# Optimization experiments

Measured on AMD Instinct MI355X. Metric: run time of the kernel, lower is better.

## Reference

```python
import jax, jax.numpy as jnp
import numpy as np

B, S, DIN, DH, NB = 4, 2048, 256, 128, 50
LN_EPS = 1e-5
THRESHOLDS = (0.5, 1.0, 2.0, 4.0)


def _layernorm(x, g, b):
    m = jnp.mean(x, axis=-1, keepdims=True)
    v = jnp.mean((x - m) ** 2, axis=-1, keepdims=True)
    return (x - m) * jax.lax.rsqrt(v + LN_EPS) * g + b


def setup_inputs() -> dict:
    key = jax.random.key(0)
    ks = jax.random.split(key, 12)
    single_repr = jax.random.normal(ks[0], (B, S, DIN), jnp.float32)
    # coordinates spread out so the <=15A local neighborhood is nontrivial
    coordinates = jax.random.normal(ks[1], (B, S, 3), jnp.float32) * 12.0
    mask = jnp.ones((B, S), jnp.float32)
    sc = 0.05
    return {
        'single_repr': single_repr,
        'coordinates': coordinates,
        'mask': mask,
        'W1': jax.random.normal(ks[2], (DIN, DH), jnp.float32) * sc,
        'b1': jnp.zeros((DH,), jnp.float32),
        'g1': jnp.ones((DH,), jnp.float32),
        'be1': jnp.zeros((DH,), jnp.float32),
        'W2': jax.random.normal(ks[3], (DH, DH), jnp.float32) * sc,
        'b2': jnp.zeros((DH,), jnp.float32),
        'g2': jnp.ones((DH,), jnp.float32),
        'be2': jnp.zeros((DH,), jnp.float32),
        'W3': jax.random.normal(ks[4], (DH, NB), jnp.float32) * sc,
        'b3': jnp.zeros((NB,), jnp.float32),
        'temperature': jnp.ones((1,), jnp.float32),
    }


def reference(single_repr, coordinates, mask, W1, b1, g1, be1, W2, b2, g2, be2, W3, b3, temperature):
    # ---- confidence MLP (dropout in eval mode = identity) ----
    h = jax.nn.relu(_layernorm(single_repr @ W1 + b1, g1, be1))
    h = jax.nn.relu(_layernorm(h @ W2 + b2, g2, be2))
    logits = (h @ W3 + b3) / temperature          # [B, S, NB]
    probs = jax.nn.softmax(logits, axis=-1)

    # ---- vectorized pLDDT (replaces the per-residue Python loop) ----
    diff = coordinates[:, :, None, :] - coordinates[:, None, :, :]   # [B,S,S,3]
    D = jnp.sqrt(jnp.sum(diff * diff, axis=-1))                      # [B,S,S]
    maskb = mask > 0.0
    local = (D <= 15.0) & maskb[:, :, None] & maskb[:, None, :]      # [B,S,S]
    counts = jnp.sum(local, axis=-1).astype(jnp.float32)             # [B,S]
    frac_sum = jnp.zeros((B, S), jnp.float32)
    for t in THRESHOLDS:  # fixed small loop over 4 thresholds
        within = jnp.sum((D <= t) & local, axis=-1).astype(jnp.float32)
        frac_sum = frac_sum + within / jnp.maximum(counts, 1.0)
    plddt = jnp.where(counts > 0, frac_sum / len(THRESHOLDS) * 100.0, 0.0)

    # ---- final masking, as in torch forward ----
    plddt = plddt * mask
    logits_m = logits * mask[:, :, None]
    probs_m = probs * mask[:, :, None]
    return plddt, logits_m, probs_m
```

## Files before the change

kernel.cpp:

```cpp
#include <hip/hip_runtime.h>
#include <float.h>
#include <math.h>

#define B_   4
#define S_   2048
#define DIN_ 256
#define DH_  128
#define NB_  50
#define NBP_ 64
#define ROWS (B_ * S_)
#define MB   16

#define MLP_BLOCKS   (ROWS / MB)
#define PLDDT_ROWSPB 32
#define PLDDT_BLOCKS (ROWS / PLDDT_ROWSPB)

typedef __attribute__((ext_vector_type(8))) short  short8;
typedef __attribute__((ext_vector_type(4))) float  f32x4;

__device__ __forceinline__ unsigned short bf16_rne(float f) {
    unsigned u = __builtin_bit_cast(unsigned, f);
    u = u + 0x7fffu + ((u >> 16) & 1u);
    return (unsigned short)(u >> 16);
}

__global__ __launch_bounds__(256) void setup_w(
    const float* __restrict__ W1, const float* __restrict__ W2,
    const float* __restrict__ W3, unsigned short* __restrict__ wt)
{
    const int t = blockIdx.x * 256 + threadIdx.x;
    const int l = t & 63, m = l & 15, kg = l >> 4;
    float src[8];
    int dst;
    if (t < 4096) {
        const int c = t >> 6, nt = c >> 3, ks = c & 7;
        const int n = nt * 16 + m, k = ks * 32 + kg * 8;
#pragma unroll
        for (int i = 0; i < 8; ++i) src[i] = W1[(k + i) * DH_ + n];
        dst = t * 8;
    } else if (t < 6144) {
        const int s = t - 4096, c = s >> 6, nt = c >> 2, ks = c & 3;
        const int n = nt * 16 + m, k = ks * 32 + kg * 8;
#pragma unroll
        for (int i = 0; i < 8; ++i) src[i] = W2[(k + i) * DH_ + n];
        dst = 32768 + s * 8;
    } else {
        const int s = t - 6144, c = s >> 6, nt = c >> 2, ks = c & 3;
        const int n = nt * 16 + m, k = ks * 32 + kg * 8;
#pragma unroll
        for (int i = 0; i < 8; ++i) src[i] = (n < NB_) ? W3[(k + i) * NB_ + n] : 0.f;
        dst = 49152 + s * 8;
    }
    union { short8 v; unsigned short u[8]; } H;
#pragma unroll
    for (int i = 0; i < 8; ++i) H.u[i] = bf16_rne(src[i]);
    *(short8*)&wt[dst] = H.v;
}

union SharedU {
    struct {
        unsigned short sA[MB * DIN_];
        float sStats[MB][20];
        float sL[MB * NBP_];
    } mlp;
    f32x4 sP[S_];
};

__global__ __launch_bounds__(512) void fused_kernel(
    const float* __restrict__ x, const float* __restrict__ coords,
    const float* __restrict__ mask,
    const float* __restrict__ b1, const float* __restrict__ g1, const float* __restrict__ be1,
    const float* __restrict__ b2, const float* __restrict__ g2, const float* __restrict__ be2,
    const float* __restrict__ b3, const float* __restrict__ temp,
    const unsigned short* __restrict__ wt,
    float* __restrict__ out_plddt,
    float* __restrict__ out_logits, float* __restrict__ out_probs)
{
    __shared__ SharedU sh;
    const int tid  = threadIdx.x;
    const int lane = tid & 63;
    const int w    = tid >> 6;

    if (blockIdx.x < MLP_BLOCKS) {
        unsigned short* sA = sh.mlp.sA;
        const int m    = lane & 15;
        const int kg   = lane >> 4;
        const int row0 = blockIdx.x * MB;

        {
            const int r  = tid >> 5;
            const int kc = (tid & 31) << 3;
            const float* xp = x + (size_t)(row0 + r) * DIN_ + kc;
            f32x4 a = *(const f32x4*)xp;
            f32x4 b = *(const f32x4*)(xp + 4);
            union { short8 v; unsigned short u[8]; } H;
#pragma unroll
            for (int i = 0; i < 8; ++i)
                H.u[i] = bf16_rne((i < 4) ? a[i] : b[i - 4]);
            const int idx = (r * 256 + kc) ^ ((r & 7) << 3);
            *(short8*)&sA[idx] = H.v;
        }
        __syncthreads();

        const int n12 = w * 16 + m;

        f32x4 aA = {0.f,0.f,0.f,0.f}, aB = {0.f,0.f,0.f,0.f};
        {
            const unsigned short* bp = wt + (w * 8) * 512;
#pragma unroll
            for (int ks = 0; ks < 8; ++ks) {
                const int ia = (m * 256 + ks * 32 + kg * 8) ^ ((m & 7) << 3);
                short8 ah = *(const short8*)&sA[ia];
                short8 bh = *(const short8*)&bp[ks * 512 + lane * 8];
                f32x4& ac = (ks & 1) ? aB : aA;
                ac = __builtin_amdgcn_mfma_f32_16x16x32_bf16(ah, bh, ac, 0, 0, 0);
            }
        }

        {
            const float bb = b1[n12], gg = g1[n12], ee = be1[n12];
            float v[4];
#pragma unroll
            for (int j = 0; j < 4; ++j) v[j] = aA[j] + aB[j] + bb;
#pragma unroll
            for (int j = 0; j < 4; ++j) {
                float sv = v[j], qv = v[j] * v[j];
                for (int off = 1; off < 16; off <<= 1) { sv += __shfl_xor(sv, off); qv += __shfl_xor(qv, off); }
                if (m == 0) { sh.mlp.sStats[kg * 4 + j][w * 2] = sv; sh.mlp.sStats[kg * 4 + j][w * 2 + 1] = qv; }
            }
            __syncthreads();
#pragma unroll
            for (int j = 0; j < 4; ++j) {
                const int r = kg * 4 + j;
                f32x4 s0 = *(const f32x4*)&sh.mlp.sStats[r][0];
                f32x4 s1 = *(const f32x4*)&sh.mlp.sStats[r][4];
                f32x4 s2 = *(const f32x4*)&sh.mlp.sStats[r][8];
                f32x4 s3 = *(const f32x4*)&sh.mlp.sStats[r][12];
                const float S = s0[0]+s0[2]+s1[0]+s1[2]+s2[0]+s2[2]+s3[0]+s3[2];
                const float Q = s0[1]+s0[3]+s1[1]+s1[3]+s2[1]+s2[3]+s3[1]+s3[3];
                const float mean = S * (1.f / DH_);
                const float inv  = rsqrtf(Q * (1.f / DH_) - mean * mean + 1e-5f);
                const float h = fmaxf(fmaf((v[j] - mean) * inv, gg, ee), 0.f);
                const int idx = (r * 128 + n12) ^ ((r & 7) << 3);
                sA[idx] = bf16_rne(h);
            }
        }
        __syncthreads();

        aA = (f32x4){0.f,0.f,0.f,0.f}; aB = (f32x4){0.f,0.f,0.f,0.f};
        {
            const unsigned short* bp = wt + 32768 + (w * 4) * 512;
#pragma unroll
            for (int ks = 0; ks < 4; ++ks) {
                const int ia = (m * 128 + ks * 32 + kg * 8) ^ ((m & 7) << 3);
                short8 ah = *(const short8*)&sA[ia];
                short8 bh = *(const short8*)&bp[ks * 512 + lane * 8];
                f32x4& ac = (ks & 1) ? aB : aA;
                ac = __builtin_amdgcn_mfma_f32_16x16x32_bf16(ah, bh, ac, 0, 0, 0);
            }
        }

        {
            const float bb = b2[n12], gg = g2[n12], ee = be2[n12];
            float v[4];
#pragma unroll
            for (int j = 0; j < 4; ++j) v[j] = aA[j] + aB[j] + bb;
#pragma unroll
            for (int j = 0; j < 4; ++j) {
                float sv = v[j], qv = v[j] * v[j];
                for (int off = 1; off < 16; off <<= 1) { sv += __shfl_xor(sv, off); qv += __shfl_xor(qv, off); }
                if (m == 0) { sh.mlp.sStats[kg * 4 + j][w * 2] = sv; sh.mlp.sStats[kg * 4 + j][w * 2 + 1] = qv; }
            }
            __syncthreads();
#pragma unroll
            for (int j = 0; j < 4; ++j) {
                const int r = kg * 4 + j;
                f32x4 s0 = *(const f32x4*)&sh.mlp.sStats[r][0];
                f32x4 s1 = *(const f32x4*)&sh.mlp.sStats[r][4];
                f32x4 s2 = *(const f32x4*)&sh.mlp.sStats[r][8];
                f32x4 s3 = *(const f32x4*)&sh.mlp.sStats[r][12];
                const float S = s0[0]+s0[2]+s1[0]+s1[2]+s2[0]+s2[2]+s3[0]+s3[2];
                const float Q = s0[1]+s0[3]+s1[1]+s1[3]+s2[1]+s2[3]+s3[1]+s3[3];
                const float mean = S * (1.f / DH_);
                const float inv  = rsqrtf(Q * (1.f / DH_) - mean * mean + 1e-5f);
                const float h = fmaxf(fmaf((v[j] - mean) * inv, gg, ee), 0.f);
                const int idx = (r * 128 + n12) ^ ((r & 7) << 3);
                sA[idx] = bf16_rne(h);
            }
        }
        __syncthreads();

        if (w < 4) {
            f32x4 cA = {0.f,0.f,0.f,0.f}, cB = {0.f,0.f,0.f,0.f};
            const unsigned short* bp = wt + 49152 + (w * 4) * 512;
#pragma unroll
            for (int ks = 0; ks < 4; ++ks) {
                const int ia = (m * 128 + ks * 32 + kg * 8) ^ ((m & 7) << 3);
                short8 ah = *(const short8*)&sA[ia];
                short8 bh = *(const short8*)&bp[ks * 512 + lane * 8];
                f32x4& ac = (ks & 1) ? cB : cA;
                ac = __builtin_amdgcn_mfma_f32_16x16x32_bf16(ah, bh, ac, 0, 0, 0);
            }
            const int n = w * 16 + m;
            const float bv = (n < NB_) ? b3[n] : 0.f;
            const float invT = 1.f / temp[0];
#pragma unroll
            for (int j = 0; j < 4; ++j)
                sh.mlp.sL[(kg * 4 + j) * NBP_ + n] = (cA[j] + cB[j] + bv) * invT;
        }
        __syncthreads();

        if (tid < 256) {
            const int r  = tid >> 4;
            const int c0 = (tid & 15) * 4;
            f32x4 lg = *(const f32x4*)&sh.mlp.sL[r * NBP_ + c0];
            float mx = -FLT_MAX;
#pragma unroll
            for (int i = 0; i < 4; ++i) if (c0 + i < NB_) mx = fmaxf(mx, lg[i]);
            for (int off = 1; off < 16; off <<= 1) mx = fmaxf(mx, __shfl_xor(mx, off));
            float e[4]; float sm = 0.f;
#pragma unroll
            for (int i = 0; i < 4; ++i) { e[i] = (c0 + i < NB_) ? expf(lg[i] - mx) : 0.f; sm += e[i]; }
            for (int off = 1; off < 16; off <<= 1) sm += __shfl_xor(sm, off);
            const float isum = 1.f / sm;
            const float mk = mask[row0 + r];
            float* ol = out_logits + (size_t)(row0 + r) * NB_;
            float* op = out_probs  + (size_t)(row0 + r) * NB_;
#pragma unroll
            for (int i = 0; i < 4; ++i) {
                const int c = c0 + i;
                if (c < NB_) { ol[c] = lg[i] * mk; op[c] = e[i] * isum * mk; }
            }
        }
    } else {
        const int pb   = blockIdx.x - MLP_BLOCKS;
        const int row0 = pb * PLDDT_ROWSPB;
        const int b    = row0 >> 11;
        const int ib0  = row0 & (S_ - 1);

        const float* cb = coords + (size_t)b * S_ * 3;
        const float* mb = mask   + (size_t)b * S_;

        {
            union { f32x4 v[3]; float f[12]; } C;
            const float* cp = cb + tid * 12;
#pragma unroll
            for (int q = 0; q < 3; ++q) C.v[q] = *(const f32x4*)(cp + q * 4);
            union { f32x4 v; float f[4]; } M;
            M.v = *(const f32x4*)(mb + tid * 4);
#pragma unroll
            for (int q = 0; q < 4; ++q)
                sh.sP[tid * 4 + q] = (f32x4){C.f[q*3], C.f[q*3+1], C.f[q*3+2], M.f[q]};
        }
        __syncthreads();

        f32x4 PI[4];
#pragma unroll
        for (int ii = 0; ii < 4; ++ii) PI[ii] = sh.sP[ib0 + w * 4 + ii];

        int cnt[4] = {0,0,0,0}, wsum[4] = {0,0,0,0};
        for (int j = lane; j < S_; j += 64) {
            const f32x4 p = sh.sP[j];
            const float gd = (p[3] > 0.f) ? 0.f : 1e30f;
#pragma unroll
            for (int ii = 0; ii < 4; ++ii) {
                const float dx = PI[ii][0] - p[0];
                const float dy = PI[ii][1] - p[1];
                const float dz = PI[ii][2] - p[2];
                const float d2 = fmaf(dx, dx, fmaf(dy, dy, dz * dz)) + gd;
                cnt[ii]  += (d2 <= 225.f);
                wsum[ii] += (d2 <= 16.f);
                wsum[ii] += (d2 <= 4.f);
                wsum[ii] += (d2 <= 1.f);
                wsum[ii] += (d2 <= 0.25f);
            }
        }
#pragma unroll
        for (int ii = 0; ii < 4; ++ii)
            for (int off = 32; off; off >>= 1) {
                cnt[ii]  += __shfl_xor(cnt[ii], off);
                wsum[ii] += __shfl_xor(wsum[ii], off);
            }
        if (lane == 0) {
#pragma unroll
            for (int ii = 0; ii < 4; ++ii) {
                const float fc = (float)cnt[ii];
                const float r  = (cnt[ii] > 0) ? (wsum[ii] * 25.f / fc) : 0.f;
                out_plddt[row0 + w * 4 + ii] = r * PI[ii][3];
            }
        }
    }
}

extern "C" void kernel_launch(void* const* d_in, const int* in_sizes, int n_in,
                              void* d_out, int out_size, void* d_ws, size_t ws_size,
                              hipStream_t stream) {
    const float* x      = (const float*)d_in[0];
    const float* coords = (const float*)d_in[1];
    const float* mask   = (const float*)d_in[2];
    const float* W1  = (const float*)d_in[3];
    const float* b1  = (const float*)d_in[4];
    const float* g1  = (const float*)d_in[5];
    const float* be1 = (const float*)d_in[6];
    const float* W2  = (const float*)d_in[7];
    const float* b2  = (const float*)d_in[8];
    const float* g2  = (const float*)d_in[9];
    const float* be2 = (const float*)d_in[10];
    const float* W3  = (const float*)d_in[11];
    const float* b3  = (const float*)d_in[12];
    const float* temp= (const float*)d_in[13];

    float* out        = (float*)d_out;
    float* out_plddt  = out;
    float* out_logits = out + (size_t)ROWS;
    float* out_probs  = out_logits + (size_t)ROWS * NB_;

    unsigned short* wt = (unsigned short*)d_ws;

    setup_w<<<28, 256, 0, stream>>>(W1, W2, W3, wt);
    fused_kernel<<<MLP_BLOCKS + PLDDT_BLOCKS, 512, 0, stream>>>(
        x, coords, mask, b1, g1, be1, b2, g2, be2, b3, temp, wt,
        out_plddt, out_logits, out_probs);
}
```

Before: 25.50 us.

## Move pLDDT into weight-setup kernel and compute threshold counts via exponent bits

The pLDDT work moves out of the fused MLP kernel and into the first kernel, next to the bf16 weight conversion. The launch bound goes from 256 to 512 threads, so 14 setup blocks replace 28. This lets the pLDDT blocks run while the weight conversion runs, and leaves the MLP kernel with a smaller grid and only its own LDS footprint. The inner distance loop now uses paired float2 FMAs and packs the count and weighted sum into one int for a single shuffle reduction. The four threshold compares become one exponent-bit computation, which depends on the thresholds being powers of four and adds a tiny epsilon to d2.

```diff
diff --git a/kernel.cpp b/kernel.cpp
--- a/kernel.cpp
+++ b/kernel.cpp
@@ -12,11 +12,13 @@
 #define MB   16
 
 #define MLP_BLOCKS   (ROWS / MB)
+#define SETUP_BLOCKS 14
 #define PLDDT_ROWSPB 32
 #define PLDDT_BLOCKS (ROWS / PLDDT_ROWSPB)
 
 typedef __attribute__((ext_vector_type(8))) short  short8;
 typedef __attribute__((ext_vector_type(4))) float  f32x4;
+typedef __attribute__((ext_vector_type(2))) float  f32x2;
 
 __device__ __forceinline__ unsigned short bf16_rne(float f) {
     unsigned u = __builtin_bit_cast(unsigned, f);
@@ -24,270 +26,278 @@
     return (unsigned short)(u >> 16);
 }
 
-__global__ __launch_bounds__(256) void setup_w(
+__global__ __launch_bounds__(512) void kernelA(
     const float* __restrict__ W1, const float* __restrict__ W2,
-    const float* __restrict__ W3, unsigned short* __restrict__ wt)
+    const float* __restrict__ W3, unsigned short* __restrict__ wt,
+    const float* __restrict__ coords, const float* __restrict__ mask,
+    float* __restrict__ out_plddt)
 {
-    const int t = blockIdx.x * 256 + threadIdx.x;
-    const int l = t & 63, m = l & 15, kg = l >> 4;
-    float src[8];
-    int dst;
-    if (t < 4096) {
-        const int c = t >> 6, nt = c >> 3, ks = c & 7;
-        const int n = nt * 16 + m, k = ks * 32 + kg * 8;
-#pragma unroll
-        for (int i = 0; i < 8; ++i) src[i] = W1[(k + i) * DH_ + n];
-        dst = t * 8;
-    } else if (t < 6144) {
-        const int s = t - 4096, c = s >> 6, nt = c >> 2, ks = c & 3;
-        const int n = nt * 16 + m, k = ks * 32 + kg * 8;
-#pragma unroll
-        for (int i = 0; i < 8; ++i) src[i] = W2[(k + i) * DH_ + n];
-        dst = 32768 + s * 8;
-    } else {
-        const int s = t - 6144, c = s >> 6, nt = c >> 2, ks = c & 3;
-        const int n = nt * 16 + m, k = ks * 32 + kg * 8;
-#pragma unroll
-        for (int i = 0; i < 8; ++i) src[i] = (n < NB_) ? W3[(k + i) * NB_ + n] : 0.f;
-        dst = 49152 + s * 8;
-    }
-    union { short8 v; unsigned short u[8]; } H;
-#pragma unroll
-    for (int i = 0; i < 8; ++i) H.u[i] = bf16_rne(src[i]);
-    *(short8*)&wt[dst] = H.v;
+    __shared__ f32x4 sP[S_];
+    const int tid = threadIdx.x;
+
+    if (blockIdx.x < SETUP_BLOCKS) {
+        const int t = blockIdx.x * 512 + tid;
+        const int l = t & 63, m = l & 15, kg = l >> 4;
+        float src[8];
+        int dst;
+        if (t < 4096) {
+            const int c = t >> 6, nt = c >> 3, ks = c & 7;
+            const int n = nt * 16 + m, k = ks * 32 + kg * 8;
+#pragma unroll
+            for (int i = 0; i < 8; ++i) src[i] = W1[(k + i) * DH_ + n];
+            dst = t * 8;
+        } else if (t < 6144) {
+            const int s = t - 4096, c = s >> 6, nt = c >> 2, ks = c & 3;
+            const int n = nt * 16 + m, k = ks * 32 + kg * 8;
+#pragma unroll
+            for (int i = 0; i < 8; ++i) src[i] = W2[(k + i) * DH_ + n];
+            dst = 32768 + s * 8;
+        } else {
+            const int s = t - 6144, c = s >> 6, nt = c >> 2, ks = c & 3;
+            const int n = nt * 16 + m, k = ks * 32 + kg * 8;
+#pragma unroll
+            for (int i = 0; i < 8; ++i) src[i] = (n < NB_) ? W3[(k + i) * NB_ + n] : 0.f;
+            dst = 49152 + s * 8;
+        }
+        union { short8 v; unsigned short u[8]; } H;
+#pragma unroll
+        for (int i = 0; i < 8; ++i) H.u[i] = bf16_rne(src[i]);
+        *(short8*)&wt[dst] = H.v;
+        return;
+    }
+
+    const int lane = tid & 63;
+    const int w    = tid >> 6;
+    const int pb   = blockIdx.x - SETUP_BLOCKS;
+    const int row0 = pb * PLDDT_ROWSPB;
+    const int b    = row0 >> 11;
+    const int ib0  = row0 & (S_ - 1);
+
+    const float* cb = coords + (size_t)b * S_ * 3;
+    const float* mb = mask   + (size_t)b * S_;
+
+    {
+        union { f32x4 v[3]; float f[12]; } C;
+        const float* cp = cb + tid * 12;
+#pragma unroll
+        for (int q = 0; q < 3; ++q) C.v[q] = *(const f32x4*)(cp + q * 4);
+        union { f32x4 v; float f[4]; } M;
+        M.v = *(const f32x4*)(mb + tid * 4);
+#pragma unroll
+        for (int q = 0; q < 4; ++q)
+            sP[tid * 4 + q] = (f32x4){C.f[q*3], C.f[q*3+1], C.f[q*3+2], M.f[q]};
+    }
+    __syncthreads();
+
+    f32x4 PI[4];
+#pragma unroll
+    for (int ii = 0; ii < 4; ++ii) PI[ii] = sP[ib0 + w * 4 + ii];
+
+    const f32x2 Px[2] = {{PI[0][0], PI[1][0]}, {PI[2][0], PI[3][0]}};
+    const f32x2 Py[2] = {{PI[0][1], PI[1][1]}, {PI[2][1], PI[3][1]}};
+    const f32x2 Pz[2] = {{PI[0][2], PI[1][2]}, {PI[2][2], PI[3][2]}};
+
+    int cnt[4] = {0,0,0,0}, ws[4] = {0,0,0,0};
+#pragma unroll 2
+    for (int j = lane; j < S_; j += 64) {
+        const f32x4 p = sP[j];
+        const float gd = (p[3] > 0.f) ? 1e-35f : 1e30f;
+        const f32x2 pg = {gd, gd};
+        const f32x2 px = {p[0], p[0]}, py = {p[1], p[1]}, pz = {p[2], p[2]};
+#pragma unroll
+        for (int pr = 0; pr < 2; ++pr) {
+            f32x2 dx = Px[pr] - px;
+            f32x2 dy = Py[pr] - py;
+            f32x2 dz = Pz[pr] - pz;
+            f32x2 d2 = __builtin_elementwise_fma(dx, dx,
+                       __builtin_elementwise_fma(dy, dy,
+                       __builtin_elementwise_fma(dz, dz, pg)));
+#pragma unroll
+            for (int el = 0; el < 2; ++el) {
+                const int ii = pr * 2 + el;
+                const float d2e = d2[el];
+                cnt[ii] += (d2e <= 225.f);
+                const unsigned u = __builtin_bit_cast(unsigned, d2e);
+                int c = (132 - (int)((u - 1u) >> 23)) >> 1;
+                c = c < 0 ? 0 : (c > 4 ? 4 : c);
+                ws[ii] += c;
+            }
+        }
+    }
+#pragma unroll
+    for (int ii = 0; ii < 4; ++ii) {
+        int acc = (cnt[ii] << 16) | ws[ii];
+        for (int off = 32; off; off >>= 1) acc += __shfl_xor(acc, off);
+        if (lane == 0) {
+            const int ct = acc >> 16, wv = acc & 0xFFFF;
+            const float r = (ct > 0) ? (wv * 25.f / (float)ct) : 0.f;
+            out_plddt[row0 + w * 4 + ii] = r * PI[ii][3];
+        }
+    }
 }
 
-union SharedU {
-    struct {
-        unsigned short sA[MB * DIN_];
-        float sStats[MB][20];
-        float sL[MB * NBP_];
-    } mlp;
-    f32x4 sP[S_];
-};
-
-__global__ __launch_bounds__(512) void fused_kernel(
-    const float* __restrict__ x, const float* __restrict__ coords,
-    const float* __restrict__ mask,
+__global__ __launch_bounds__(512) void kernelB(
+    const float* __restrict__ x, const float* __restrict__ mask,
     const float* __restrict__ b1, const float* __restrict__ g1, const float* __restrict__ be1,
     const float* __restrict__ b2, const float* __restrict__ g2, const float* __restrict__ be2,
     const float* __restrict__ b3, const float* __restrict__ temp,
     const unsigned short* __restrict__ wt,
-    float* __restrict__ out_plddt,
     float* __restrict__ out_logits, float* __restrict__ out_probs)
 {
-    __shared__ SharedU sh;
+    __shared__ unsigned short sA[MB * DIN_];
+    __shared__ float sStats[MB][20];
+    __shared__ float sL[MB * NBP_];
+
     const int tid  = threadIdx.x;
     const int lane = tid & 63;
     const int w    = tid >> 6;
-
-    if (blockIdx.x < MLP_BLOCKS) {
-        unsigned short* sA = sh.mlp.sA;
-        const int m    = lane & 15;
-        const int kg   = lane >> 4;
-        const int row0 = blockIdx.x * MB;
-
-        {
-            const int r  = tid >> 5;
-            const int kc = (tid & 31) << 3;
-            const float* xp = x + (size_t)(row0 + r) * DIN_ + kc;
-            f32x4 a = *(const f32x4*)xp;
-            f32x4 b = *(const f32x4*)(xp + 4);
-            union { short8 v; unsigned short u[8]; } H;
-#pragma unroll
-            for (int i = 0; i < 8; ++i)
-                H.u[i] = bf16_rne((i < 4) ? a[i] : b[i - 4]);
-            const int idx = (r * 256 + kc) ^ ((r & 7) << 3);
-            *(short8*)&sA[idx] = H.v;
+    const int m    = lane & 15;
+    const int kg   = lane >> 4;
+    const int row0 = blockIdx.x * MB;
+
+    {
+        const int r  = tid >> 5;
+        const int kc = (tid & 31) << 3;
+        const float* xp = x + (size_t)(row0 + r) * DIN_ + kc;
+        f32x4 a = *(const f32x4*)xp;
+        f32x4 b = *(const f32x4*)(xp + 4);
+        union { short8 v; unsigned short u[8]; } H;
+#pragma unroll
+        for (int i = 0; i < 8; ++i)
+            H.u[i] = bf16_rne((i < 4) ? a[i] : b[i - 4]);
+        const int idx = (r * 256 + kc) ^ ((r & 7) << 3);
+        *(short8*)&sA[idx] = H.v;
+    }
+    __syncthreads();
+
+    const int n12 = w * 16 + m;
+
+    f32x4 aA = {0,0,0,0}, aB = {0,0,0,0};
+    {
+        const unsigned short* bp = wt + (w * 8) * 512;
+#pragma unroll
+        for (int ks = 0; ks < 8; ++ks) {
+            const int ia = (m * 256 + ks * 32 + kg * 8) ^ ((m & 7) << 3);
+            short8 ah = *(const short8*)&sA[ia];
+            short8 bh = *(const short8*)&bp[ks * 512 + lane * 8];
+            f32x4& ac = (ks & 1) ? aB : aA;
+            ac = __builtin_amdgcn_mfma_f32_16x16x32_bf16(ah, bh, ac, 0, 0, 0);
+        }
+    }
+
+    {
+        const float bb = b1[n12], gg = g1[n12], ee = be1[n12];
+        float v[4];
+#pragma unroll
+        for (int j = 0; j < 4; ++j) v[j] = aA[j] + aB[j] + bb;
+#pragma unroll
+        for (int j = 0; j < 4; ++j) {
+            float sv = v[j], qv = v[j] * v[j];
+            for (int off = 1; off < 16; off <<= 1) { sv += __shfl_xor(sv, off); qv += __shfl_xor(qv, off); }
+            if (m == 0) { sStats[kg * 4 + j][w * 2] = sv; sStats[kg * 4 + j][w * 2 + 1] = qv; }
         }
         __syncthreads();
-
-        const int n12 = w * 16 + m;
-
-        f32x4 aA = {0.f,0.f,0.f,0.f}, aB = {0.f,0.f,0.f,0.f};
-        {
-            const unsigned short* bp = wt + (w * 8) * 512;
-#pragma unroll
-            for (int ks = 0; ks < 8; ++ks) {
-                const int ia = (m * 256 + ks * 32 + kg * 8) ^ ((m & 7) << 3);
-                short8 ah = *(const short8*)&sA[ia];
-                short8 bh = *(const short8*)&bp[ks * 512 + lane * 8];
-                f32x4& ac = (ks & 1) ? aB : aA;
-                ac = __builtin_amdgcn_mfma_f32_16x16x32_bf16(ah, bh, ac, 0, 0, 0);
-            }
-        }
-
-        {
-            const float bb = b1[n12], gg = g1[n12], ee = be1[n12];
-            float v[4];
-#pragma unroll
-            for (int j = 0; j < 4; ++j) v[j] = aA[j] + aB[j] + bb;
-#pragma unroll
-            for (int j = 0; j < 4; ++j) {
-                float sv = v[j], qv = v[j] * v[j];
-                for (int off = 1; off < 16; off <<= 1) { sv += __shfl_xor(sv, off); qv += __shfl_xor(qv, off); }
-                if (m == 0) { sh.mlp.sStats[kg * 4 + j][w * 2] = sv; sh.mlp.sStats[kg * 4 + j][w * 2 + 1] = qv; }
-            }
-            __syncthreads();
-#pragma unroll
-            for (int j = 0; j < 4; ++j) {
-                const int r = kg * 4 + j;
-                f32x4 s0 = *(const f32x4*)&sh.mlp.sStats[r][0];
-                f32x4 s1 = *(const f32x4*)&sh.mlp.sStats[r][4];
-                f32x4 s2 = *(const f32x4*)&sh.mlp.sStats[r][8];
-                f32x4 s3 = *(const f32x4*)&sh.mlp.sStats[r][12];
-                const float S = s0[0]+s0[2]+s1[0]+s1[2]+s2[0]+s2[2]+s3[0]+s3[2];
-                const float Q = s0[1]+s0[3]+s1[1]+s1[3]+s2[1]+s2[3]+s3[1]+s3[3];
-                const float mean = S * (1.f / DH_);
-                const float inv  = rsqrtf(Q * (1.f / DH_) - mean * mean + 1e-5f);
-                const float h = fmaxf(fmaf((v[j] - mean) * inv, gg, ee), 0.f);
-                const int idx = (r * 128 + n12) ^ ((r & 7) << 3);
-                sA[idx] = bf16_rne(h);
-            }
+#pragma unroll
+        for (int j = 0; j < 4; ++j) {
+            const int r = kg * 4 + j;
+            f32x4 s0 = *(const f32x4*)&sStats[r][0];
+            f32x4 s1 = *(const f32x4*)&sStats[r][4];
+            f32x4 s2 = *(const f32x4*)&sStats[r][8];
+            f32x4 s3 = *(const f32x4*)&sStats[r][12];
+            const float S = s0[0]+s0[2]+s1[0]+s1[2]+s2[0]+s2[2]+s3[0]+s3[2];
+            const float Q = s0[1]+s0[3]+s1[1]+s1[3]+s2[1]+s2[3]+s3[1]+s3[3];
+            const float mean = S * (1.f / DH_);
+            const float inv  = rsqrtf(Q * (1.f / DH_) - mean * mean + 1e-5f);
+            const float h = fmaxf(fmaf((v[j] - mean) * inv, gg, ee), 0.f);
+            const int idx = (r * 128 + n12) ^ ((r & 7) << 3);
+            sA[idx] = bf16_rne(h);
+        }
+    }
+    __syncthreads();
+
+    aA = (f32x4){0,0,0,0}; aB = (f32x4){0,0,0,0};
+    {
+        const unsigned short* bp = wt + 32768 + (w * 4) * 512;
+#pragma unroll
+        for (int ks = 0; ks < 4; ++ks) {
+            const int ia = (m * 128 + ks * 32 + kg * 8) ^ ((m & 7) << 3);
+            short8 ah = *(const short8*)&sA[ia];
+            short8 bh = *(const short8*)&bp[ks * 512 + lane * 8];
+            f32x4& ac = (ks & 1) ? aB : aA;
+            ac = __builtin_amdgcn_mfma_f32_16x16x32_bf16(ah, bh, ac, 0, 0, 0);
+        }
+    }
+
+    {
+        const float bb = b2[n12], gg = g2[n12], ee = be2[n12];
+        float v[4];
+#pragma unroll
+        for (int j = 0; j < 4; ++j) v[j] = aA[j] + aB[j] + bb;
+#pragma unroll
+        for (int j = 0; j < 4; ++j) {
+            float sv = v[j], qv = v[j] * v[j];
+            for (int off = 1; off < 16; off <<= 1) { sv += __shfl_xor(sv, off); qv += __shfl_xor(qv, off); }
+            if (m == 0) { sStats[kg * 4 + j][w * 2] = sv; sStats[kg * 4 + j][w * 2 + 1] = qv; }
         }
         __syncthreads();
-
-        aA = (f32x4){0.f,0.f,0.f,0.f}; aB = (f32x4){0.f,0.f,0.f,0.f};
-        {
-            const unsigned short* bp = wt + 32768 + (w * 4) * 512;
-#pragma unroll
-            for (int ks = 0; ks < 4; ++ks) {
-                const int ia = (m * 128 + ks * 32 + kg * 8) ^ ((m & 7) << 3);
-                short8 ah = *(const short8*)&sA[ia];
-                short8 bh = *(const short8*)&bp[ks * 512 + lane * 8];
-                f32x4& ac = (ks & 1) ? aB : aA;
-                ac = __builtin_amdgcn_mfma_f32_16x16x32_bf16(ah, bh, ac, 0, 0, 0);
-            }
-        }
-
-        {
-            const float bb = b2[n12], gg = g2[n12], ee = be2[n12];
-            float v[4];
-#pragma unroll
-            for (int j = 0; j < 4; ++j) v[j] = aA[j] + aB[j] + bb;
-#pragma unroll
-            for (int j = 0; j < 4; ++j) {
-                float sv = v[j], qv = v[j] * v[j];
-                for (int off = 1; off < 16; off <<= 1) { sv += __shfl_xor(sv, off); qv += __shfl_xor(qv, off); }
-                if (m == 0) { sh.mlp.sStats[kg * 4 + j][w * 2] = sv; sh.mlp.sStats[kg * 4 + j][w * 2 + 1] = qv; }
-            }
-            __syncthreads();
-#pragma unroll
-            for (int j = 0; j < 4; ++j) {
-                const int r = kg * 4 + j;
-                f32x4 s0 = *(const f32x4*)&sh.mlp.sStats[r][0];
-                f32x4 s1 = *(const f32x4*)&sh.mlp.sStats[r][4];
-                f32x4 s2 = *(const f32x4*)&sh.mlp.sStats[r][8];
-                f32x4 s3 = *(const f32x4*)&sh.mlp.sStats[r][12];
-                const float S = s0[0]+s0[2]+s1[0]+s1[2]+s2[0]+s2[2]+s3[0]+s3[2];
-                const float Q = s0[1]+s0[3]+s1[1]+s1[3]+s2[1]+s2[3]+s3[1]+s3[3];
-                const float mean = S * (1.f / DH_);
-                const float inv  = rsqrtf(Q * (1.f / DH_) - mean * mean + 1e-5f);
-                const float h = fmaxf(fmaf((v[j] - mean) * inv, gg, ee), 0.f);
-                const int idx = (r * 128 + n12) ^ ((r & 7) << 3);
-                sA[idx] = bf16_rne(h);
-            }
-        }
-        __syncthreads();
-
-        if (w < 4) {
-            f32x4 cA = {0.f,0.f,0.f,0.f}, cB = {0.f,0.f,0.f,0.f};
-            const unsigned short* bp = wt + 49152 + (w * 4) * 512;
-#pragma unroll
-            for (int ks = 0; ks < 4; ++ks) {
-                const int ia = (m * 128 + ks * 32 + kg * 8) ^ ((m & 7) << 3);
-                short8 ah = *(const short8*)&sA[ia];
-                short8 bh = *(const short8*)&bp[ks * 512 + lane * 8];
-                f32x4& ac = (ks & 1) ? cB : cA;
-                ac = __builtin_amdgcn_mfma_f32_16x16x32_bf16(ah, bh, ac, 0, 0, 0);
-            }
-            const int n = w * 16 + m;
-            const float bv = (n < NB_) ? b3[n] : 0.f;
-            const float invT = 1.f / temp[0];
-#pragma unroll
-            for (int j = 0; j < 4; ++j)
-                sh.mlp.sL[(kg * 4 + j) * NBP_ + n] = (cA[j] + cB[j] + bv) * invT;
-        }
-        __syncthreads();
-
-        if (tid < 256) {
-            const int r  = tid >> 4;
-            const int c0 = (tid & 15) * 4;
-            f32x4 lg = *(const f32x4*)&sh.mlp.sL[r * NBP_ + c0];
-            float mx = -FLT_MAX;
-#pragma unroll
-            for (int i = 0; i < 4; ++i) if (c0 + i < NB_) mx = fmaxf(mx, lg[i]);
-            for (int off = 1; off < 16; off <<= 1) mx = fmaxf(mx, __shfl_xor(mx, off));
-            float e[4]; float sm = 0.f;
-#pragma unroll
-            for (int i = 0; i < 4; ++i) { e[i] = (c0 + i < NB_) ? expf(lg[i] - mx) : 0.f; sm += e[i]; }
-            for (int off = 1; off < 16; off <<= 1) sm += __shfl_xor(sm, off);
-            const float isum = 1.f / sm;
-            const float mk = mask[row0 + r];
-            float* ol = out_logits + (size_t)(row0 + r) * NB_;
-            float* op = out_probs  + (size_t)(row0 + r) * NB_;
-#pragma unroll
-            for (int i = 0; i < 4; ++i) {
-                const int c = c0 + i;
-                if (c < NB_) { ol[c] = lg[i] * mk; op[c] = e[i] * isum * mk; }
-            }
-        }
-    } else {
-        const int pb   = blockIdx.x - MLP_BLOCKS;
-        const int row0 = pb * PLDDT_ROWSPB;
-        const int b    = row0 >> 11;
-        const int ib0  = row0 & (S_ - 1);
-
-        const float* cb = coords + (size_t)b * S_ * 3;
-        const float* mb = mask   + (size_t)b * S_;
-
-        {
-            union { f32x4 v[3]; float f[12]; } C;
-            const float* cp = cb + tid * 12;
-#pragma unroll
-            for (int q = 0; q < 3; ++q) C.v[q] = *(const f32x4*)(cp + q * 4);
-            union { f32x4 v; float f[4]; } M;
-            M.v = *(const f32x4*)(mb + tid * 4);
-#pragma unroll
-            for (int q = 0; q < 4; ++q)
-                sh.sP[tid * 4 + q] = (f32x4){C.f[q*3], C.f[q*3+1], C.f[q*3+2], M.f[q]};
-        }
-        __syncthreads();
-
-        f32x4 PI[4];
-#pragma unroll
-        for (int ii = 0; ii < 4; ++ii) PI[ii] = sh.sP[ib0 + w * 4 + ii];
-
-        int cnt[4] = {0,0,0,0}, wsum[4] = {0,0,0,0};
-        for (int j = lane; j < S_; j += 64) {
-            const f32x4 p = sh.sP[j];
-            const float gd = (p[3] > 0.f) ? 0.f : 1e30f;
-#pragma unroll
-            for (int ii = 0; ii < 4; ++ii) {
-                const float dx = PI[ii][0] - p[0];
-                const float dy = PI[ii][1] - p[1];
-                const float dz = PI[ii][2] - p[2];
-                const float d2 = fmaf(dx, dx, fmaf(dy, dy, dz * dz)) + gd;
-                cnt[ii]  += (d2 <= 225.f);
-                wsum[ii] += (d2 <= 16.f);
-                wsum[ii] += (d2 <= 4.f);
-                wsum[ii] += (d2 <= 1.f);
-                wsum[ii] += (d2 <= 0.25f);
-            }
-        }
-#pragma unroll
-        for (int ii = 0; ii < 4; ++ii)
-            for (int off = 32; off; off >>= 1) {
-                cnt[ii]  += __shfl_xor(cnt[ii], off);
-                wsum[ii] += __shfl_xor(wsum[ii], off);
-            }
-        if (lane == 0) {
-#pragma unroll
-            for (int ii = 0; ii < 4; ++ii) {
-                const float fc = (float)cnt[ii];
-                const float r  = (cnt[ii] > 0) ? (wsum[ii] * 25.f / fc) : 0.f;
-                out_plddt[row0 + w * 4 + ii] = r * PI[ii][3];
-            }
+#pragma unroll
+        for (int j = 0; j < 4; ++j) {
+            const int r = kg * 4 + j;
+            f32x4 s0 = *(const f32x4*)&sStats[r][0];
+            f32x4 s1 = *(const f32x4*)&sStats[r][4];
+            f32x4 s2 = *(const f32x4*)&sStats[r][8];
+            f32x4 s3 = *(const f32x4*)&sStats[r][12];
+            const float S = s0[0]+s0[2]+s1[0]+s1[2]+s2[0]+s2[2]+s3[0]+s3[2];
+            const float Q = s0[1]+s0[3]+s1[1]+s1[3]+s2[1]+s2[3]+s3[1]+s3[3];
+            const float mean = S * (1.f / DH_);
+            const float inv  = rsqrtf(Q * (1.f / DH_) - mean * mean + 1e-5f);
+            const float h = fmaxf(fmaf((v[j] - mean) * inv, gg, ee), 0.f);
+            const int idx = (r * 128 + n12) ^ ((r & 7) << 3);
+            sA[idx] = bf16_rne(h);
+        }
+    }
+    __syncthreads();
+
+    if (w < 4) {
+        f32x4 cA = {0,0,0,0}, cB = {0,0,0,0};
+        const unsigned short* bp = wt + 49152 + (w * 4) * 512;
+#pragma unroll
+        for (int ks = 0; ks < 4; ++ks) {
+            const int ia = (m * 128 + ks * 32 + kg * 8) ^ ((m & 7) << 3);
+            short8 ah = *(const short8*)&sA[ia];
+            short8 bh = *(const short8*)&bp[ks * 512 + lane * 8];
+            f32x4& ac = (ks & 1) ? cB : cA;
+            ac = __builtin_amdgcn_mfma_f32_16x16x32_bf16(ah, bh, ac, 0, 0, 0);
+        }
+        const int n = w * 16 + m;
+        const float bv = (n < NB_) ? b3[n] : 0.f;
+        const float invT = 1.f / temp[0];
+#pragma unroll
+        for (int j = 0; j < 4; ++j)
+            sL[(kg * 4 + j) * NBP_ + n] = (cA[j] + cB[j] + bv) * invT;
+    }
+    __syncthreads();
+
+    if (tid < 256) {
+        const int r  = tid >> 4;
+        const int c0 = (tid & 15) * 4;
+        f32x4 lg = *(const f32x4*)&sL[r * NBP_ + c0];
+        float mx = -FLT_MAX;
+#pragma unroll
+        for (int i = 0; i < 4; ++i) if (c0 + i < NB_) mx = fmaxf(mx, lg[i]);
+        for (int off = 1; off < 16; off <<= 1) mx = fmaxf(mx, __shfl_xor(mx, off));
+        float e[4]; float sm = 0.f;
+#pragma unroll
+        for (int i = 0; i < 4; ++i) { e[i] = (c0 + i < NB_) ? expf(lg[i] - mx) : 0.f; sm += e[i]; }
+        for (int off = 1; off < 16; off <<= 1) sm += __shfl_xor(sm, off);
+        const float isum = 1.f / sm;
+        const float mk = mask[row0 + r];
+        float* ol = out_logits + (size_t)(row0 + r) * NB_;
+        float* op = out_probs  + (size_t)(row0 + r) * NB_;
+#pragma unroll
+        for (int i = 0; i < 4; ++i) {
+            const int c = c0 + i;
+            if (c < NB_) { ol[c] = lg[i] * mk; op[c] = e[i] * isum * mk; }
         }
     }
 }
@@ -317,8 +327,8 @@
 
     unsigned short* wt = (unsigned short*)d_ws;
 
-    setup_w<<<28, 256, 0, stream>>>(W1, W2, W3, wt);
-    fused_kernel<<<MLP_BLOCKS + PLDDT_BLOCKS, 512, 0, stream>>>(
-        x, coords, mask, b1, g1, be1, b2, g2, be2, b3, temp, wt,
-        out_plddt, out_logits, out_probs);
+    kernelA<<<SETUP_BLOCKS + PLDDT_BLOCKS, 512, 0, stream>>>(
+        W1, W2, W3, wt, coords, mask, out_plddt);
+    kernelB<<<MLP_BLOCKS, 512, 0, stream>>>(
+        x, mask, b1, g1, be1, b2, g2, be2, b3, temp, wt, out_logits, out_probs);
 }
```

Measured after the change: 23.90 us, median of 3. -6.3%, faster.

## Reorder pLDDT blocks first and compute threshold counts via exponent bit trick

Applied to the files above, without the earlier changes.

Puts the pLDDT blocks ahead of the MLP blocks in the grid so the heavier O(S^2) distance work is dispatched first. It packs two query residues into float2 for packed FMA distance computation. It replaces the four threshold comparisons with an exponent-field formula, since the thresholds are powers of four. It also packs count and within-sum into one int so the wave reduction needs half the shuffles, and launches setup with 512-thread blocks. The exponent trick relies on exact boundary behaviour and the tiny 1e-35 offset, and the 16-bit packing limits each count to 65535.

```diff
diff --git a/kernel.cpp b/kernel.cpp
--- a/kernel.cpp
+++ b/kernel.cpp
@@ -11,12 +11,14 @@
 #define ROWS (B_ * S_)
 #define MB   16
 
-#define MLP_BLOCKS   (ROWS / MB)
+#define SETUP_BLOCKS 14
 #define PLDDT_ROWSPB 32
 #define PLDDT_BLOCKS (ROWS / PLDDT_ROWSPB)
+#define MLP_BLOCKS   (ROWS / MB)
 
 typedef __attribute__((ext_vector_type(8))) short  short8;
 typedef __attribute__((ext_vector_type(4))) float  f32x4;
+typedef __attribute__((ext_vector_type(2))) float  f32x2;
 
 __device__ __forceinline__ unsigned short bf16_rne(float f) {
     unsigned u = __builtin_bit_cast(unsigned, f);
@@ -24,11 +26,11 @@
     return (unsigned short)(u >> 16);
 }
 
-__global__ __launch_bounds__(256) void setup_w(
+__global__ __launch_bounds__(512) void setup_w(
     const float* __restrict__ W1, const float* __restrict__ W2,
     const float* __restrict__ W3, unsigned short* __restrict__ wt)
 {
-    const int t = blockIdx.x * 256 + threadIdx.x;
+    const int t = blockIdx.x * 512 + threadIdx.x;
     const int l = t & 63, m = l & 15, kg = l >> 4;
     float src[8];
     int dst;
@@ -81,11 +83,78 @@
     const int lane = tid & 63;
     const int w    = tid >> 6;
 
-    if (blockIdx.x < MLP_BLOCKS) {
+    if (blockIdx.x < PLDDT_BLOCKS) {
+        const int pb   = blockIdx.x;
+        const int row0 = pb * PLDDT_ROWSPB;
+        const int b    = row0 >> 11;
+        const int ib0  = row0 & (S_ - 1);
+
+        const float* cb = coords + (size_t)b * S_ * 3;
+        const float* mb = mask   + (size_t)b * S_;
+
+        {
+            union { f32x4 v[3]; float f[12]; } C;
+            const float* cp = cb + tid * 12;
+#pragma unroll
+            for (int q = 0; q < 3; ++q) C.v[q] = *(const f32x4*)(cp + q * 4);
+            union { f32x4 v; float f[4]; } M;
+            M.v = *(const f32x4*)(mb + tid * 4);
+#pragma unroll
+            for (int q = 0; q < 4; ++q)
+                sh.sP[tid * 4 + q] = (f32x4){C.f[q*3], C.f[q*3+1], C.f[q*3+2], M.f[q]};
+        }
+        __syncthreads();
+
+        f32x4 PI[4];
+#pragma unroll
+        for (int ii = 0; ii < 4; ++ii) PI[ii] = sh.sP[ib0 + w * 4 + ii];
+
+        const f32x2 Px[2] = {{PI[0][0], PI[1][0]}, {PI[2][0], PI[3][0]}};
+        const f32x2 Py[2] = {{PI[0][1], PI[1][1]}, {PI[2][1], PI[3][1]}};
+        const f32x2 Pz[2] = {{PI[0][2], PI[1][2]}, {PI[2][2], PI[3][2]}};
+
+        int cnt[4] = {0,0,0,0}, ws[4] = {0,0,0,0};
+#pragma unroll 2
+        for (int j = lane; j < S_; j += 64) {
+            const f32x4 p = sh.sP[j];
+            const float gd = (p[3] > 0.f) ? 1e-35f : 1e30f;
+            const f32x2 pg = {gd, gd};
+            const f32x2 px = {p[0], p[0]}, py = {p[1], p[1]}, pz = {p[2], p[2]};
+#pragma unroll
+            for (int pr = 0; pr < 2; ++pr) {
+                f32x2 dx = Px[pr] - px;
+                f32x2 dy = Py[pr] - py;
+                f32x2 dz = Pz[pr] - pz;
+                f32x2 d2 = __builtin_elementwise_fma(dx, dx,
+                           __builtin_elementwise_fma(dy, dy,
+                           __builtin_elementwise_fma(dz, dz, pg)));
+#pragma unroll
+                for (int el = 0; el < 2; ++el) {
+                    const int ii = pr * 2 + el;
+                    const float d2e = d2[el];
+                    cnt[ii] += (d2e <= 225.f);
+                    const unsigned u = __builtin_bit_cast(unsigned, d2e);
+                    int c = (132 - (int)((u - 1u) >> 23)) >> 1;
+                    c = c < 0 ? 0 : (c > 4 ? 4 : c);
+                    ws[ii] += c;
+                }
+            }
+        }
+#pragma unroll
+        for (int ii = 0; ii < 4; ++ii) {
+            int acc = (cnt[ii] << 16) | ws[ii];
+            for (int off = 32; off; off >>= 1) acc += __shfl_xor(acc, off);
+            if (lane == 0) {
+                const int ct = acc >> 16, wv = acc & 0xFFFF;
+                const float r = (ct > 0) ? (wv * 25.f / (float)ct) : 0.f;
+                out_plddt[row0 + w * 4 + ii] = r * PI[ii][3];
+            }
+        }
+    } else {
         unsigned short* sA = sh.mlp.sA;
         const int m    = lane & 15;
         const int kg   = lane >> 4;
-        const int row0 = blockIdx.x * MB;
+        const int row0 = (blockIdx.x - PLDDT_BLOCKS) * MB;
 
         {
             const int r  = tid >> 5;
@@ -104,7 +173,7 @@
 
         const int n12 = w * 16 + m;
 
-        f32x4 aA = {0.f,0.f,0.f,0.f}, aB = {0.f,0.f,0.f,0.f};
+        f32x4 aA = {0,0,0,0}, aB = {0,0,0,0};
         {
             const unsigned short* bp = wt + (w * 8) * 512;
 #pragma unroll
@@ -147,7 +216,7 @@
         }
         __syncthreads();
 
-        aA = (f32x4){0.f,0.f,0.f,0.f}; aB = (f32x4){0.f,0.f,0.f,0.f};
+        aA = (f32x4){0,0,0,0}; aB = (f32x4){0,0,0,0};
         {
             const unsigned short* bp = wt + 32768 + (w * 4) * 512;
 #pragma unroll
@@ -191,7 +260,7 @@
         __syncthreads();
 
         if (w < 4) {
-            f32x4 cA = {0.f,0.f,0.f,0.f}, cB = {0.f,0.f,0.f,0.f};
+            f32x4 cA = {0,0,0,0}, cB = {0,0,0,0};
             const unsigned short* bp = wt + 49152 + (w * 4) * 512;
 #pragma unroll
             for (int ks = 0; ks < 4; ++ks) {
@@ -230,63 +299,6 @@
             for (int i = 0; i < 4; ++i) {
                 const int c = c0 + i;
                 if (c < NB_) { ol[c] = lg[i] * mk; op[c] = e[i] * isum * mk; }
-            }
-        }
-    } else {
-        const int pb   = blockIdx.x - MLP_BLOCKS;
-        const int row0 = pb * PLDDT_ROWSPB;
-        const int b    = row0 >> 11;
-        const int ib0  = row0 & (S_ - 1);
-
-        const float* cb = coords + (size_t)b * S_ * 3;
-        const float* mb = mask   + (size_t)b * S_;
-
-        {
-            union { f32x4 v[3]; float f[12]; } C;
-            const float* cp = cb + tid * 12;
-#pragma unroll
-            for (int q = 0; q < 3; ++q) C.v[q] = *(const f32x4*)(cp + q * 4);
-            union { f32x4 v; float f[4]; } M;
-            M.v = *(const f32x4*)(mb + tid * 4);
-#pragma unroll
-            for (int q = 0; q < 4; ++q)
-                sh.sP[tid * 4 + q] = (f32x4){C.f[q*3], C.f[q*3+1], C.f[q*3+2], M.f[q]};
-        }
-        __syncthreads();
-
-        f32x4 PI[4];
-#pragma unroll
-        for (int ii = 0; ii < 4; ++ii) PI[ii] = sh.sP[ib0 + w * 4 + ii];
-
-        int cnt[4] = {0,0,0,0}, wsum[4] = {0,0,0,0};
-        for (int j = lane; j < S_; j += 64) {
-            const f32x4 p = sh.sP[j];
-            const float gd = (p[3] > 0.f) ? 0.f : 1e30f;
-#pragma unroll
-            for (int ii = 0; ii < 4; ++ii) {
-                const float dx = PI[ii][0] - p[0];
-                const float dy = PI[ii][1] - p[1];
-                const float dz = PI[ii][2] - p[2];
-                const float d2 = fmaf(dx, dx, fmaf(dy, dy, dz * dz)) + gd;
-                cnt[ii]  += (d2 <= 225.f);
-                wsum[ii] += (d2 <= 16.f);
-                wsum[ii] += (d2 <= 4.f);
-                wsum[ii] += (d2 <= 1.f);
-                wsum[ii] += (d2 <= 0.25f);
-            }
-        }
-#pragma unroll
-        for (int ii = 0; ii < 4; ++ii)
-            for (int off = 32; off; off >>= 1) {
-                cnt[ii]  += __shfl_xor(cnt[ii], off);
-                wsum[ii] += __shfl_xor(wsum[ii], off);
-            }
-        if (lane == 0) {
-#pragma unroll
-            for (int ii = 0; ii < 4; ++ii) {
-                const float fc = (float)cnt[ii];
-                const float r  = (cnt[ii] > 0) ? (wsum[ii] * 25.f / fc) : 0.f;
-                out_plddt[row0 + w * 4 + ii] = r * PI[ii][3];
             }
         }
     }
@@ -317,8 +329,8 @@
 
     unsigned short* wt = (unsigned short*)d_ws;
 
-    setup_w<<<28, 256, 0, stream>>>(W1, W2, W3, wt);
-    fused_kernel<<<MLP_BLOCKS + PLDDT_BLOCKS, 512, 0, stream>>>(
+    setup_w<<<SETUP_BLOCKS, 512, 0, stream>>>(W1, W2, W3, wt);
+    fused_kernel<<<PLDDT_BLOCKS + MLP_BLOCKS, 512, 0, stream>>>(
         x, coords, mask, b1, g1, be1, b2, g2, be2, b3, temp, wt,
         out_plddt, out_logits, out_probs);
 }
```

Measured after the change: 24.15 us. 1.06x faster.
